# Optimization experiments

Hardware: AMD Instinct MI355X
Metric: run time of the kernel (lower is better)

The kernel has to match this reference:

```python
import jax, jax.numpy as jnp
import numpy as np

REG = 0.01
NUM_PS, NUM_QS, NUM_RS, D = 100000, 100000, 1000, 256
B = 4096


def setup_inputs() -> dict:
    key = jax.random.key(0)
    k1, k2, k3, k4, k5, k6, k7 = jax.random.split(key, 7)
    # xavier_uniform bound for a (d, d*d) fan view: sqrt(6/(d + d*d))
    bound = float(np.sqrt(6.0 / (D + D * D)))
    return {
        "ps": jax.random.randint(k1, (B,), 0, NUM_PS),
        "qs": jax.random.randint(k2, (B,), 0, NUM_QS),
        "rs": jax.random.randint(k3, (B,), 0, NUM_RS),
        "P_table": jax.random.normal(k4, (NUM_PS, D), dtype=jnp.float32),
        "Q_table": jax.random.normal(k5, (NUM_QS, D), dtype=jnp.float32),
        "R_table": jax.random.normal(k6, (NUM_RS, D), dtype=jnp.float32),
        "W": jax.random.uniform(k7, (D, D, D), dtype=jnp.float32, minval=-bound, maxval=bound),
    }


def reference(ps, qs, rs, P_table, Q_table, R_table, W):
    p = P_table[ps]  # (B, d)
    q = Q_table[qs]  # (B, d)
    r = R_table[rs]  # (B, d)
    # W.view(d, d*d) then reshape (B, d_r, d_q): axis order of W is (p, r, q)
    # trilinear: out_b = sum_{i,j,k} p_bi W_ijk r_bj q_bk
    Wp = jnp.einsum('bi,ijk->bjk', p, W)        # (B, d, d), the big GEMM
    out = jnp.einsum('bjk,bj,bk->b', Wp, r, q)  # two batched mat-vecs
    inferences = out[:, None]                   # (B, 1)
    regs = REG * (jnp.linalg.norm(p) + jnp.linalg.norm(q) + jnp.linalg.norm(r))
    return inferences, regs
```

## Files before the change

kernel.cpp:

```cpp
#include <hip/hip_runtime.h>
#include <hip/hip_bf16.h>


#define DDIM 256
#define NIK  65536
#define BM   128
#define BN   128
#define BK   64
#define NCH2 2
#define NPANEL 8

typedef unsigned int uint;
typedef __attribute__((ext_vector_type(8))) short bf16x8;
typedef __attribute__((ext_vector_type(4))) float f32x4;

static __device__ __forceinline__ unsigned short f2bf(float f) {
    __hip_bfloat16 h = __float2bfloat16(f);
    return *reinterpret_cast<unsigned short*>(&h);
}
static __device__ __forceinline__ float bf2f(unsigned short u) {
    return __uint_as_float(((uint)u) << 16);
}

#define GLOAD_LDS16(gsrc, ldst)                                                \
    __builtin_amdgcn_global_load_lds(                                          \
        (const __attribute__((address_space(1))) void*)(gsrc),                 \
        (__attribute__((address_space(3))) void*)(ldst), 16, 0, 0)

__global__ __launch_bounds__(256)
void conv_r_kernel(const float* __restrict__ R, unsigned short* __restrict__ Rb,
                   int n4) {
    int idx = blockIdx.x * 256 + threadIdx.x;
    if (idx < n4) {
        float4 v = *reinterpret_cast<const float4*>(R + idx * 4);
        ushort4 o;
        o.x = f2bf(v.x); o.y = f2bf(v.y); o.z = f2bf(v.z); o.w = f2bf(v.w);
        *reinterpret_cast<ushort4*>(Rb + idx * 4) = o;
    }
}

__global__ __launch_bounds__(256)
void conv_wt_kernel(const float* __restrict__ W, unsigned short* __restrict__ Wt) {
    const int k0 = blockIdx.x * 64;
    const int j0 = blockIdx.y * 128;
    const int i  = blockIdx.z;
    const int t  = threadIdx.x;

    __shared__ float sT[64][129];

    const float* Wi = W + (size_t)i * NIK;
#pragma unroll
    for (int it = 0; it < 8; ++it) {
        int slot = it * 256 + t;
        int jj = slot >> 4, c = slot & 15;
        float4 v = *reinterpret_cast<const float4*>(
            Wi + (size_t)(j0 + jj) * DDIM + k0 + c * 4);
        sT[c * 4 + 0][jj] = v.x;
        sT[c * 4 + 1][jj] = v.y;
        sT[c * 4 + 2][jj] = v.z;
        sT[c * 4 + 3][jj] = v.w;
    }
    __syncthreads();
#pragma unroll
    for (int it = 0; it < 4; ++it) {
        int u = it * 256 + t;
        int kk = u >> 4, jg = u & 15;
        union { unsigned short us[8]; uint4 v; } pk;
#pragma unroll
        for (int m = 0; m < 8; ++m) pk.us[m] = f2bf(sT[kk][jg * 8 + m]);
        *reinterpret_cast<uint4*>(
            Wt + (size_t)(i * DDIM + k0 + kk) * DDIM + j0 + jg * 8) = pk.v;
    }
}

__global__ __launch_bounds__(256, 2)
void stage1_kernel(const unsigned short* __restrict__ Rb,
                   const unsigned short* __restrict__ Wt,
                   unsigned short* __restrict__ WR,
                   int r_lo, int cnt) {
    const int t     = threadIdx.x;
    const int lane  = t & 63;
    const int wid   = t >> 6;
    const int strip = blockIdx.x;
    const int r0    = blockIdx.y * BM;

    __shared__ char smem[65536];

    const int wr = (wid >> 1) * 64;
    const int wn = (wid & 1) * 64;

    f32x4 acc[4][4];
#pragma unroll
    for (int a = 0; a < 4; ++a)
#pragma unroll
        for (int b = 0; b < 4; ++b) {
            acc[a][b][0] = 0.f; acc[a][b][1] = 0.f;
            acc[a][b][2] = 0.f; acc[a][b][3] = 0.f;
        }

#define STAGE_S(s, boff)                                                        \
    {                                                                           \
        const int j0s = ((s) & 3) * BK;                                         \
        const int n0s = strip * (BN * NPANEL) + ((s) >> 2) * BN;                \
        _Pragma("unroll")                                                       \
        for (int c = 0; c < 4; ++c) {                                           \
            int u = c * 256 + t;                                                \
            int row = u >> 3, g = u & 7;                                        \
            int rg = r0 + row;                                                  \
            if (rg >= cnt) rg = 0;                                              \
            GLOAD_LDS16(Rb + (size_t)(r_lo + rg) * DDIM + j0s +                 \
                            ((g ^ (row & 7)) << 3),                             \
                        smem + (boff) + u * 16);                                \
        }                                                                       \
        _Pragma("unroll")                                                       \
        for (int c = 0; c < 4; ++c) {                                           \
            int u = c * 256 + t;                                                \
            int row = u >> 3, g = u & 7;                                        \
            GLOAD_LDS16(Wt + (size_t)(n0s + row) * DDIM + j0s +                 \
                            ((g ^ (row & 7)) << 3),                             \
                        smem + 32768 + (boff) + u * 16);                        \
        }                                                                       \
    }

    STAGE_S(0, 0);
    __syncthreads();

    const int c16   = lane & 15;
    const int gq    = lane >> 4;
    const int ubase = wn >> 5;
    char* WRb = (char*)WR;

    for (int s = 0; s < 4 * NPANEL; ++s) {
        const int coff = (s & 1) << 14;
        if (s < 4 * NPANEL - 1) STAGE_S(s + 1, coff ^ 16384);

        char* Acur = smem + coff;
        char* Bcur = smem + 32768 + coff;
#pragma unroll
        for (int ks = 0; ks < 2; ++ks) {
            bf16x8 a[4], b[4];
            const int jg = ks * 4 + (lane >> 4);
#pragma unroll
            for (int f = 0; f < 4; ++f) {
                int rowB = wn + f * 16 + (lane & 15);
                a[f] = *reinterpret_cast<const bf16x8*>(
                    Bcur + rowB * 128 + ((jg ^ (rowB & 7)) << 4));
                int rowA = wr + f * 16 + (lane & 15);
                b[f] = *reinterpret_cast<const bf16x8*>(
                    Acur + rowA * 128 + ((jg ^ (rowA & 7)) << 4));
            }
#pragma unroll
            for (int fi = 0; fi < 4; ++fi)
#pragma unroll
                for (int fr = 0; fr < 4; ++fr)
                    acc[fi][fr] = __builtin_amdgcn_mfma_f32_16x16x32_bf16(
                        a[fi], b[fr], acc[fi][fr], 0, 0, 0);
        }

        if ((s & 3) == 3) {
            const int n0  = strip * (BN * NPANEL) + (s >> 2) * BN;
            const int i_g = n0 >> 8;
            const size_t obase = (size_t)(i_g >> 4) * 8192 +
                                 (size_t)(i_g & 15) * 512 +
                                 (size_t)(n0 & 255) * 2;
#pragma unroll
            for (int fr = 0; fr < 4; ++fr) {
                int rg = r0 + wr + fr * 16 + c16;
                if (rg < cnt) {
#pragma unroll
                    for (int kts = 0; kts < 2; ++kts) {
                        union { unsigned short us[8]; uint4 v; } pk;
#pragma unroll
                        for (int vv = 0; vv < 4; ++vv) {
                            pk.us[vv]     = f2bf(acc[2 * kts + 0][fr][vv]);
                            pk.us[4 + vv] = f2bf(acc[2 * kts + 1][fr][vv]);
                        }
                        *reinterpret_cast<uint4*>(
                            WRb + (size_t)rg * 131072 + obase +
                            (ubase + kts) * 64 + gq * 16) = pk.v;
                    }
                }
            }
#pragma unroll
            for (int a = 0; a < 4; ++a)
#pragma unroll
                for (int b = 0; b < 4; ++b) {
                    acc[a][b][0] = 0.f; acc[a][b][1] = 0.f;
                    acc[a][b][2] = 0.f; acc[a][b][3] = 0.f;
                }
        }
        __syncthreads();
    }
#undef STAGE_S
}

__global__ void prep_kernel(int* __restrict__ counts, float* __restrict__ norms,
                            int n) {
    int idx = blockIdx.x * 256 + threadIdx.x;
    if (idx < n) counts[idx] = 0;
    if (idx < 3) norms[idx] = 0.f;
}

__global__ void hist_kernel(const int* __restrict__ rs, int* __restrict__ counts,
                            int B) {
    int b = blockIdx.x * 256 + threadIdx.x;
    if (b < B) atomicAdd(&counts[rs[b]], 1);
}

__global__ __launch_bounds__(1024)
void scan_kernel(const int* __restrict__ counts, int* __restrict__ offs,
                 int* __restrict__ cursor, int n) {
    __shared__ int buf[2][1024];
    const int t = threadIdx.x;
    int cur = 0;
    buf[0][t] = (t < n) ? counts[t] : 0;
    __syncthreads();
    for (int d = 1; d < 1024; d <<= 1) {
        int x = buf[cur][t] + ((t >= d) ? buf[cur][t - d] : 0);
        buf[cur ^ 1][t] = x;
        cur ^= 1;
        __syncthreads();
    }
    if (t < n) {
        int inc = buf[cur][t];
        offs[t + 1] = inc;
        cursor[t] = inc - counts[t];
        if (t == 0) offs[0] = 0;
    }
}

__global__ void fill_kernel(const int* __restrict__ rs, int* __restrict__ cursor,
                            int* __restrict__ list, int B) {
    int b = blockIdx.x * 256 + threadIdx.x;
    if (b < B) {
        int pos = atomicAdd(&cursor[rs[b]], 1);
        list[pos] = b;
    }
}

__global__ __launch_bounds__(256)
void stage2_kernel(const int* __restrict__ list, const int* __restrict__ offs,
                   const int* __restrict__ ps, const int* __restrict__ qs,
                   const float* __restrict__ P, const float* __restrict__ Q,
                   const unsigned short* __restrict__ WR,
                   float* __restrict__ partial, int r_lo, int B) {
    const int r_rel = blockIdx.x;
    const int r     = r_lo + r_rel;
    const int start = offs[r], end = offs[r + 1];
    if (start >= end) return;
    const int ihalf = blockIdx.y;
    const int t     = threadIdx.x;
    const int lane  = t & 63;
    const int w     = t >> 6;
    const int s     = lane & 15;
    const int kg    = lane >> 4;

    __shared__ float Lq[16][258];
    __shared__ float Lp[16][133];
    __shared__ float red[16][4];

    const unsigned short* Mbase = WR + (size_t)r_rel * NIK;

    for (int s0 = start; s0 < end; s0 += 16) {
        const int ns = min(16, end - s0);
        for (int u = t; u < ns * 64; u += 256) {
            int ss = u >> 6, c = u & 63;
            *reinterpret_cast<float4*>(&Lq[ss][c * 4]) =
                *reinterpret_cast<const float4*>(
                    Q + (size_t)qs[list[s0 + ss]] * DDIM + c * 4);
        }
        for (int u = t; u < ns * 32; u += 256) {
            int ss = u >> 5, c = u & 31;
            *reinterpret_cast<float4*>(&Lp[ss][c * 4]) =
                *reinterpret_cast<const float4*>(
                    P + (size_t)ps[list[s0 + ss]] * DDIM + ihalf * 128 + c * 4);
        }
        __syncthreads();

        bf16x8 bq[8];
#pragma unroll
        for (int kt = 0; kt < 8; ++kt) {
#pragma unroll
            for (int eh = 0; eh < 2; ++eh) {
#pragma unroll
                for (int ev = 0; ev < 4; ++ev) {
                    float v = (s < ns) ? Lq[s][kt * 32 + eh * 16 + kg * 4 + ev]
                                       : 0.f;
                    bq[kt][eh * 4 + ev] = (short)f2bf(v);
                }
            }
        }

        float acc_out = 0.f;
#pragma unroll
        for (int ibl = 0; ibl < 2; ++ibl) {
            const int ibh = w * 2 + ibl;
            const int ibg = ihalf * 8 + ibh;
            const unsigned short* abase =
                Mbase + (size_t)ibg * 4096 + (lane & 15) * 256 + kg * 8;
            bf16x8 af[8];
#pragma unroll
            for (int kt = 0; kt < 8; ++kt)
                af[kt] = *reinterpret_cast<const bf16x8*>(abase + kt * 32);
            f32x4 acc = {0.f, 0.f, 0.f, 0.f};
#pragma unroll
            for (int kt = 0; kt < 8; ++kt)
                acc = __builtin_amdgcn_mfma_f32_16x16x32_bf16(af[kt], bq[kt],
                                                              acc, 0, 0, 0);
#pragma unroll
            for (int reg = 0; reg < 4; ++reg) {
                int il = ibh * 16 + kg * 4 + reg;
                float pv = (s < ns) ? Lp[s][il] : 0.f;
                acc_out += acc[reg] * pv;
            }
        }
        acc_out += __shfl_xor(acc_out, 16, 64);
        acc_out += __shfl_xor(acc_out, 32, 64);
        if (lane < 16) red[s][w] = acc_out;
        __syncthreads();
        if (t < ns)
            partial[(size_t)ihalf * B + list[s0 + t]] =
                red[t][0] + red[t][1] + red[t][2] + red[t][3];
        __syncthreads();
    }
}

__global__ void sum_out_kernel(const float* __restrict__ partial,
                               float* __restrict__ out, int B) {
    int b = blockIdx.x * 256 + threadIdx.x;
    if (b < B) out[b] = partial[b] + partial[(size_t)B + b];
}

__global__ __launch_bounds__(256)
void norm_kernel(const int* __restrict__ ps, const int* __restrict__ qs,
                 const int* __restrict__ rs, const float* __restrict__ P,
                 const float* __restrict__ Q, const float* __restrict__ R,
                 float* __restrict__ accum, int B) {
    const int which = blockIdx.y;
    const int*   idx = (which == 0) ? ps : (which == 1) ? qs : rs;
    const float* tab = (which == 0) ? P : (which == 1) ? Q : R;
    float a = 0.f;
    const int total = B * 64;
    for (int e = blockIdx.x * 256 + threadIdx.x; e < total; e += gridDim.x * 256) {
        int b = e >> 6, cc = e & 63;
        float4 v = *reinterpret_cast<const float4*>(tab + (size_t)idx[b] * DDIM + cc * 4);
        a += v.x * v.x + v.y * v.y + v.z * v.z + v.w * v.w;
    }
#pragma unroll
    for (int off = 32; off; off >>= 1) a += __shfl_down(a, off, 64);
    __shared__ float red[4];
    if ((threadIdx.x & 63) == 0) red[threadIdx.x >> 6] = a;
    __syncthreads();
    if (threadIdx.x == 0) atomicAdd(accum + which, red[0] + red[1] + red[2] + red[3]);
}

__global__ void finalize_kernel(const float* __restrict__ n,
                                float* __restrict__ out, int nB) {
    if (threadIdx.x == 0 && blockIdx.x == 0)
        out[nB] = 0.01f * (sqrtf(n[0]) + sqrtf(n[1]) + sqrtf(n[2]));
}

extern "C" void kernel_launch(void* const* d_in, const int* in_sizes, int n_in,
                              void* d_out, int out_size, void* d_ws,
                              size_t ws_size, hipStream_t stream) {
    const int*   ps = (const int*)d_in[0];
    const int*   qs = (const int*)d_in[1];
    const int*   rs = (const int*)d_in[2];
    const float* P  = (const float*)d_in[3];
    const float* Q  = (const float*)d_in[4];
    const float* R  = (const float*)d_in[5];
    const float* W  = (const float*)d_in[6];
    float* out = (float*)d_out;

    const int B      = in_sizes[0];
    const int NUM_RS = in_sizes[5] / DDIM;

    size_t off = 0;
    float* norms = (float*)((char*)d_ws + off);          off += 256;
    int* counts  = (int*)((char*)d_ws + off);            off += (size_t)NUM_RS * 4;
    int* offs    = (int*)((char*)d_ws + off);            off += (size_t)(NUM_RS + 1) * 4;
    int* cursor  = (int*)((char*)d_ws + off);            off += (size_t)NUM_RS * 4;
    int* list    = (int*)((char*)d_ws + off);            off += (size_t)B * 4;
    off = (off + 255) & ~(size_t)255;
    float* partial = (float*)((char*)d_ws + off);        off += (size_t)NCH2 * B * 4;
    off = (off + 255) & ~(size_t)255;
    unsigned short* Rb = (unsigned short*)((char*)d_ws + off);
    off += (size_t)NUM_RS * DDIM * 2;
    off = (off + 255) & ~(size_t)255;
    unsigned short* Wt = (unsigned short*)((char*)d_ws + off);
    off += (size_t)NIK * DDIM * 2;
    off = (off + 255) & ~(size_t)255;
    unsigned short* WR = (unsigned short*)((char*)d_ws + off);

    size_t wr_bytes = (ws_size > off) ? ws_size - off : 0;
    int max_chunk = (int)(wr_bytes / ((size_t)NIK * 2));
    if (max_chunk > NUM_RS) max_chunk = NUM_RS;
    if (max_chunk < 1) max_chunk = 1;

    prep_kernel<<<(NUM_RS + 255) / 256, 256, 0, stream>>>(counts, norms, NUM_RS);
    hist_kernel<<<(B + 255) / 256, 256, 0, stream>>>(rs, counts, B);
    scan_kernel<<<1, 1024, 0, stream>>>(counts, offs, cursor, NUM_RS);
    fill_kernel<<<(B + 255) / 256, 256, 0, stream>>>(rs, cursor, list, B);
    norm_kernel<<<dim3(128, 3), 256, 0, stream>>>(ps, qs, rs, P, Q, R, norms, B);
    finalize_kernel<<<1, 64, 0, stream>>>(norms, out, B);

    conv_r_kernel<<<(NUM_RS * DDIM / 4 + 255) / 256, 256, 0, stream>>>(
        R, Rb, NUM_RS * DDIM / 4);
    conv_wt_kernel<<<dim3(4, 2, DDIM), 256, 0, stream>>>(W, Wt);

    for (int lo = 0; lo < NUM_RS; lo += max_chunk) {
        int cnt = NUM_RS - lo;
        if (cnt > max_chunk) cnt = max_chunk;
        dim3 g1(NIK / BN / NPANEL, (cnt + BM - 1) / BM);
        stage1_kernel<<<g1, 256, 0, stream>>>(Rb, Wt, WR, lo, cnt);
        stage2_kernel<<<dim3(cnt, NCH2), 256, 0, stream>>>(
            list, offs, ps, qs, P, Q, WR, partial, lo, B);
    }
    sum_out_kernel<<<(B + 255) / 256, 256, 0, stream>>>(partial, out, B);
}
```

Before: 128.4 us.

## Fuse the trilinear contraction into the GEMM epilogue and drop the WR intermediate

The separate stage2 kernel and the large bf16 WR buffer are removed. The GEMM epilogue now stages each finished accumulator tile in LDS. Each thread then reduces its assigned batch elements (from the r-sorted list) against pre-gathered Q and P rows, writing per-strip partial sums that a final kernel adds up. This avoids writing and re-reading the full per-r W·r tensor and the chunk loop that depended on workspace size. In exchange the epilogue gains extra barriers, scalar dot loops with uneven per-thread work, and a new gather kernel for Q and P.

```diff
diff --git a/kernel.cpp b/kernel.cpp
--- a/kernel.cpp
+++ b/kernel.cpp
@@ -7,8 +7,9 @@
 #define BM   128
 #define BN   128
 #define BK   64
-#define NCH2 2
 #define NPANEL 8
+#define NSTRIP 64
+#define MAXS 8
 
 typedef unsigned int uint;
 typedef __attribute__((ext_vector_type(8))) short bf16x8;
@@ -37,6 +38,16 @@
         o.x = f2bf(v.x); o.y = f2bf(v.y); o.z = f2bf(v.z); o.w = f2bf(v.w);
         *reinterpret_cast<ushort4*>(Rb + idx * 4) = o;
     }
+}
+
+__global__ __launch_bounds__(256)
+void conv_qp_kernel(const int* __restrict__ qs, const int* __restrict__ ps,
+                    const float* __restrict__ Q, const float* __restrict__ P,
+                    float* __restrict__ Qb, float* __restrict__ Pb) {
+    const int b = blockIdx.x;
+    const int t = threadIdx.x;
+    Qb[(size_t)b * DDIM + t] = Q[(size_t)qs[b] * DDIM + t];
+    Pb[(size_t)b * DDIM + t] = P[(size_t)ps[b] * DDIM + t];
 }
 
 __global__ __launch_bounds__(256)
@@ -76,8 +87,10 @@
 __global__ __launch_bounds__(256, 2)
 void stage1_kernel(const unsigned short* __restrict__ Rb,
                    const unsigned short* __restrict__ Wt,
-                   unsigned short* __restrict__ WR,
-                   int r_lo, int cnt) {
+                   const int* __restrict__ rs, const int* __restrict__ list,
+                   const int* __restrict__ offs,
+                   const float* __restrict__ Qb, const float* __restrict__ Pb,
+                   float* __restrict__ partial, int cnt) {
     const int t     = threadIdx.x;
     const int lane  = t & 63;
     const int wid   = t >> 6;
@@ -85,9 +98,27 @@
     const int r0    = blockIdx.y * BM;
 
     __shared__ char smem[65536];
-
-    const int wr = (wid >> 1) * 64;
-    const int wn = (wid & 1) * 64;
+    __shared__ unsigned short eplds[2 * 4096];
+
+    const int wr  = (wid >> 1) * 64;
+    const int wn  = (wid & 1) * 64;
+    const int c16 = lane & 15;
+    const int gq  = lane >> 4;
+
+    const int start = offs[r0];
+    int rend = r0 + BM; if (rend > cnt) rend = cnt;
+    const int end = offs[rend];
+    int   meta[MAXS];
+    float racc[MAXS];
+#pragma unroll
+    for (int sl = 0; sl < MAXS; ++sl) {
+        int idx = start + t + sl * 256;
+        if (idx < end) {
+            int b = list[idx];
+            meta[sl] = b | ((rs[b] - r0) << 16);
+        } else meta[sl] = -1;
+        racc[sl] = 0.f;
+    }
 
     f32x4 acc[4][4];
 #pragma unroll
@@ -108,7 +139,7 @@
             int row = u >> 3, g = u & 7;                                        \
             int rg = r0 + row;                                                  \
             if (rg >= cnt) rg = 0;                                              \
-            GLOAD_LDS16(Rb + (size_t)(r_lo + rg) * DDIM + j0s +                 \
+            GLOAD_LDS16(Rb + (size_t)rg * DDIM + j0s +                          \
                             ((g ^ (row & 7)) << 3),                             \
                         smem + (boff) + u * 16);                                \
         }                                                                       \
@@ -125,11 +156,6 @@
     STAGE_S(0, 0);
     __syncthreads();
 
-    const int c16   = lane & 15;
-    const int gq    = lane >> 4;
-    const int ubase = wn >> 5;
-    char* WRb = (char*)WR;
-
     for (int s = 0; s < 4 * NPANEL; ++s) {
         const int coff = (s & 1) << 14;
         if (s < 4 * NPANEL - 1) STAGE_S(s + 1, coff ^ 16384);
@@ -158,26 +184,52 @@
         }
 
         if ((s & 3) == 3) {
-            const int n0  = strip * (BN * NPANEL) + (s >> 2) * BN;
-            const int i_g = n0 >> 8;
-            const size_t obase = (size_t)(i_g >> 4) * 8192 +
-                                 (size_t)(i_g & 15) * 512 +
-                                 (size_t)(n0 & 255) * 2;
-#pragma unroll
-            for (int fr = 0; fr < 4; ++fr) {
-                int rg = r0 + wr + fr * 16 + c16;
-                if (rg < cnt) {
-#pragma unroll
-                    for (int kts = 0; kts < 2; ++kts) {
-                        union { unsigned short us[8]; uint4 v; } pk;
-#pragma unroll
-                        for (int vv = 0; vv < 4; ++vv) {
-                            pk.us[vv]     = f2bf(acc[2 * kts + 0][fr][vv]);
-                            pk.us[4 + vv] = f2bf(acc[2 * kts + 1][fr][vv]);
+            const int n0    = strip * (BN * NPANEL) + (s >> 2) * BN;
+            const int i_g   = n0 >> 8;
+            const int khalf = (n0 >> 7) & 1;
+            const float* qbase = Qb + khalf * 128;
+#pragma unroll
+            for (int qt = 0; qt < 4; ++qt) {
+                unsigned short* ep = eplds + (qt & 1) * 4096;
+                if ((wr >> 6) == (qt >> 1)) {
+#pragma unroll
+                    for (int f2 = 0; f2 < 2; ++f2) {
+                        const int fr = (qt & 1) * 2 + f2;
+                        const int rl = f2 * 16 + c16;
+#pragma unroll
+                        for (int fi = 0; fi < 4; ++fi) {
+                            const int ggr = (wn >> 2) + fi * 4 + gq;
+                            union { unsigned short us[4]; uint2 v; } pk;
+#pragma unroll
+                            for (int vv = 0; vv < 4; ++vv)
+                                pk.us[vv] = f2bf(acc[fi][fr][vv]);
+                            *reinterpret_cast<uint2*>(
+                                ep + rl * 128 + ((ggr ^ rl) << 2)) = pk.v;
                         }
-                        *reinterpret_cast<uint4*>(
-                            WRb + (size_t)rg * 131072 + obase +
-                            (ubase + kts) * 64 + gq * 16) = pk.v;
+                    }
+                }
+                __syncthreads();
+#pragma unroll
+                for (int sl = 0; sl < MAXS; ++sl) {
+                    int m = meta[sl];
+                    if (m >= 0 && (m >> 21) == qt) {
+                        const int b  = m & 0xFFFF;
+                        const int rl = (m >> 16) & 31;
+                        const unsigned short* tp = ep + rl * 128;
+                        const float* qp = qbase + (size_t)b * DDIM;
+                        float dot = 0.f;
+                        for (int g = 0; g < 32; ++g) {
+                            union { unsigned short us[4]; uint2 v; } tv;
+                            tv.v = *reinterpret_cast<const uint2*>(
+                                tp + ((g ^ rl) << 2));
+                            float4 qv = *reinterpret_cast<const float4*>(
+                                qp + g * 4);
+                            dot += bf2f(tv.us[0]) * qv.x +
+                                   bf2f(tv.us[1]) * qv.y +
+                                   bf2f(tv.us[2]) * qv.z +
+                                   bf2f(tv.us[3]) * qv.w;
+                        }
+                        racc[sl] += Pb[(size_t)b * DDIM + i_g] * dot;
                     }
                 }
             }
@@ -191,6 +243,11 @@
         }
         __syncthreads();
     }
+
+#pragma unroll
+    for (int sl = 0; sl < MAXS; ++sl)
+        if (meta[sl] >= 0)
+            partial[(size_t)(meta[sl] & 0xFFFF) * NSTRIP + strip] = racc[sl];
 #undef STAGE_S
 }
 
@@ -239,96 +296,20 @@
 }
 
 __global__ __launch_bounds__(256)
-void stage2_kernel(const int* __restrict__ list, const int* __restrict__ offs,
-                   const int* __restrict__ ps, const int* __restrict__ qs,
-                   const float* __restrict__ P, const float* __restrict__ Q,
-                   const unsigned short* __restrict__ WR,
-                   float* __restrict__ partial, int r_lo, int B) {
-    const int r_rel = blockIdx.x;
-    const int r     = r_lo + r_rel;
-    const int start = offs[r], end = offs[r + 1];
-    if (start >= end) return;
-    const int ihalf = blockIdx.y;
-    const int t     = threadIdx.x;
-    const int lane  = t & 63;
-    const int w     = t >> 6;
-    const int s     = lane & 15;
-    const int kg    = lane >> 4;
-
-    __shared__ float Lq[16][258];
-    __shared__ float Lp[16][133];
-    __shared__ float red[16][4];
-
-    const unsigned short* Mbase = WR + (size_t)r_rel * NIK;
-
-    for (int s0 = start; s0 < end; s0 += 16) {
-        const int ns = min(16, end - s0);
-        for (int u = t; u < ns * 64; u += 256) {
-            int ss = u >> 6, c = u & 63;
-            *reinterpret_cast<float4*>(&Lq[ss][c * 4]) =
-                *reinterpret_cast<const float4*>(
-                    Q + (size_t)qs[list[s0 + ss]] * DDIM + c * 4);
+void sum_out_kernel(const float* __restrict__ partial, float* __restrict__ out,
+                    int B) {
+    int b = blockIdx.x * 256 + threadIdx.x;
+    if (b < B) {
+        const float4* p4 =
+            reinterpret_cast<const float4*>(partial + (size_t)b * NSTRIP);
+        float s = 0.f;
+#pragma unroll
+        for (int i = 0; i < NSTRIP / 4; ++i) {
+            float4 v = p4[i];
+            s += (v.x + v.y) + (v.z + v.w);
         }
-        for (int u = t; u < ns * 32; u += 256) {
-            int ss = u >> 5, c = u & 31;
-            *reinterpret_cast<float4*>(&Lp[ss][c * 4]) =
-                *reinterpret_cast<const float4*>(
-                    P + (size_t)ps[list[s0 + ss]] * DDIM + ihalf * 128 + c * 4);
-        }
-        __syncthreads();
-
-        bf16x8 bq[8];
-#pragma unroll
-        for (int kt = 0; kt < 8; ++kt) {
-#pragma unroll
-            for (int eh = 0; eh < 2; ++eh) {
-#pragma unroll
-                for (int ev = 0; ev < 4; ++ev) {
-                    float v = (s < ns) ? Lq[s][kt * 32 + eh * 16 + kg * 4 + ev]
-                                       : 0.f;
-                    bq[kt][eh * 4 + ev] = (short)f2bf(v);
-                }
-            }
-        }
-
-        float acc_out = 0.f;
-#pragma unroll
-        for (int ibl = 0; ibl < 2; ++ibl) {
-            const int ibh = w * 2 + ibl;
-            const int ibg = ihalf * 8 + ibh;
-            const unsigned short* abase =
-                Mbase + (size_t)ibg * 4096 + (lane & 15) * 256 + kg * 8;
-            bf16x8 af[8];
-#pragma unroll
-            for (int kt = 0; kt < 8; ++kt)
-                af[kt] = *reinterpret_cast<const bf16x8*>(abase + kt * 32);
-            f32x4 acc = {0.f, 0.f, 0.f, 0.f};
-#pragma unroll
-            for (int kt = 0; kt < 8; ++kt)
-                acc = __builtin_amdgcn_mfma_f32_16x16x32_bf16(af[kt], bq[kt],
-                                                              acc, 0, 0, 0);
-#pragma unroll
-            for (int reg = 0; reg < 4; ++reg) {
-                int il = ibh * 16 + kg * 4 + reg;
-                float pv = (s < ns) ? Lp[s][il] : 0.f;
-                acc_out += acc[reg] * pv;
-            }
-        }
-        acc_out += __shfl_xor(acc_out, 16, 64);
-        acc_out += __shfl_xor(acc_out, 32, 64);
-        if (lane < 16) red[s][w] = acc_out;
-        __syncthreads();
-        if (t < ns)
-            partial[(size_t)ihalf * B + list[s0 + t]] =
-                red[t][0] + red[t][1] + red[t][2] + red[t][3];
-        __syncthreads();
-    }
-}
-
-__global__ void sum_out_kernel(const float* __restrict__ partial,
-                               float* __restrict__ out, int B) {
-    int b = blockIdx.x * 256 + threadIdx.x;
-    if (b < B) out[b] = partial[b] + partial[(size_t)B + b];
+        out[b] = s;
+    }
 }
 
 __global__ __launch_bounds__(256)
@@ -382,20 +363,16 @@
     int* cursor  = (int*)((char*)d_ws + off);            off += (size_t)NUM_RS * 4;
     int* list    = (int*)((char*)d_ws + off);            off += (size_t)B * 4;
     off = (off + 255) & ~(size_t)255;
-    float* partial = (float*)((char*)d_ws + off);        off += (size_t)NCH2 * B * 4;
+    float* partial = (float*)((char*)d_ws + off);        off += (size_t)B * NSTRIP * 4;
+    off = (off + 255) & ~(size_t)255;
+    float* Qb = (float*)((char*)d_ws + off);             off += (size_t)B * DDIM * 4;
+    float* Pb = (float*)((char*)d_ws + off);             off += (size_t)B * DDIM * 4;
     off = (off + 255) & ~(size_t)255;
     unsigned short* Rb = (unsigned short*)((char*)d_ws + off);
     off += (size_t)NUM_RS * DDIM * 2;
     off = (off + 255) & ~(size_t)255;
     unsigned short* Wt = (unsigned short*)((char*)d_ws + off);
     off += (size_t)NIK * DDIM * 2;
-    off = (off + 255) & ~(size_t)255;
-    unsigned short* WR = (unsigned short*)((char*)d_ws + off);
-
-    size_t wr_bytes = (ws_size > off) ? ws_size - off : 0;
-    int max_chunk = (int)(wr_bytes / ((size_t)NIK * 2));
-    if (max_chunk > NUM_RS) max_chunk = NUM_RS;
-    if (max_chunk < 1) max_chunk = 1;
 
     prep_kernel<<<(NUM_RS + 255) / 256, 256, 0, stream>>>(counts, norms, NUM_RS);
     hist_kernel<<<(B + 255) / 256, 256, 0, stream>>>(rs, counts, B);
@@ -406,15 +383,12 @@
 
     conv_r_kernel<<<(NUM_RS * DDIM / 4 + 255) / 256, 256, 0, stream>>>(
         R, Rb, NUM_RS * DDIM / 4);
+    conv_qp_kernel<<<B, 256, 0, stream>>>(qs, ps, Q, P, Qb, Pb);
     conv_wt_kernel<<<dim3(4, 2, DDIM), 256, 0, stream>>>(W, Wt);
 
-    for (int lo = 0; lo < NUM_RS; lo += max_chunk) {
-        int cnt = NUM_RS - lo;
-        if (cnt > max_chunk) cnt = max_chunk;
-        dim3 g1(NIK / BN / NPANEL, (cnt + BM - 1) / BM);
-        stage1_kernel<<<g1, 256, 0, stream>>>(Rb, Wt, WR, lo, cnt);
-        stage2_kernel<<<dim3(cnt, NCH2), 256, 0, stream>>>(
-            list, offs, ps, qs, P, Q, WR, partial, lo, B);
-    }
+    dim3 g1(NSTRIP, (NUM_RS + BM - 1) / BM);
+    stage1_kernel<<<g1, 256, 0, stream>>>(Rb, Wt, rs, list, offs, Qb, Pb,
+                                          partial, NUM_RS);
+
     sum_out_kernel<<<(B + 255) / 256, 256, 0, stream>>>(partial, out, B);
 }
```

New measurement: 422.4 us. 3.29x slower.

## Hoist R operand fragments into registers once per block in stage1

Applied to the files above, without the earlier changes.

The R tile for the block's rows is loaded once through shared memory into 32 bf16x8 register fragments, covering all four K slices. The main loop then streams only W panels through double-buffered LDS, halving shared memory and dropping the repeated R global loads and LDS reads on every step. In exchange, 128 extra VGPRs per thread are held live, which under launch_bounds(256,2) may cause spills or limit occupancy.

```diff
diff --git a/kernel.cpp b/kernel.cpp
--- a/kernel.cpp
+++ b/kernel.cpp
@@ -84,10 +84,41 @@
     const int strip = blockIdx.x;
     const int r0    = blockIdx.y * BM;
 
-    __shared__ char smem[65536];
+    __shared__ char smem[32768];
 
     const int wr = (wid >> 1) * 64;
     const int wn = (wid & 1) * 64;
+
+    bf16x8 rfrag[8][4];
+    {
+#pragma unroll
+        for (int rd = 0; rd < 4; ++rd) {
+            const int j0s = rd * BK;
+            __syncthreads();
+#pragma unroll
+            for (int c = 0; c < 4; ++c) {
+                int u = c * 256 + t;
+                int row = u >> 3, g = u & 7;
+                int rg = r0 + row;
+                if (rg >= cnt) rg = 0;
+                GLOAD_LDS16(Rb + (size_t)(r_lo + rg) * DDIM + j0s +
+                                ((g ^ (row & 7)) << 3),
+                            smem + u * 16);
+            }
+            __syncthreads();
+#pragma unroll
+            for (int ks = 0; ks < 2; ++ks) {
+                const int jg = ks * 4 + (lane >> 4);
+#pragma unroll
+                for (int f = 0; f < 4; ++f) {
+                    int rowA = wr + f * 16 + (lane & 15);
+                    rfrag[rd * 2 + ks][f] = *reinterpret_cast<const bf16x8*>(
+                        smem + rowA * 128 + ((jg ^ (rowA & 7)) << 4));
+                }
+            }
+        }
+        __syncthreads();
+    }
 
     f32x4 acc[4][4];
 #pragma unroll
@@ -98,31 +129,21 @@
             acc[a][b][2] = 0.f; acc[a][b][3] = 0.f;
         }
 
-#define STAGE_S(s, boff)                                                        \
+#define STAGE_W(p, kt, boff)                                                    \
     {                                                                           \
-        const int j0s = ((s) & 3) * BK;                                         \
-        const int n0s = strip * (BN * NPANEL) + ((s) >> 2) * BN;                \
-        _Pragma("unroll")                                                       \
-        for (int c = 0; c < 4; ++c) {                                           \
-            int u = c * 256 + t;                                                \
-            int row = u >> 3, g = u & 7;                                        \
-            int rg = r0 + row;                                                  \
-            if (rg >= cnt) rg = 0;                                              \
-            GLOAD_LDS16(Rb + (size_t)(r_lo + rg) * DDIM + j0s +                 \
-                            ((g ^ (row & 7)) << 3),                             \
-                        smem + (boff) + u * 16);                                \
-        }                                                                       \
+        const int j0s = (kt) * BK;                                              \
+        const int n0s = strip * (BN * NPANEL) + (p) * BN;                       \
         _Pragma("unroll")                                                       \
         for (int c = 0; c < 4; ++c) {                                           \
             int u = c * 256 + t;                                                \
             int row = u >> 3, g = u & 7;                                        \
             GLOAD_LDS16(Wt + (size_t)(n0s + row) * DDIM + j0s +                 \
                             ((g ^ (row & 7)) << 3),                             \
-                        smem + 32768 + (boff) + u * 16);                        \
+                        smem + (boff) + u * 16);                                \
         }                                                                       \
     }
 
-    STAGE_S(0, 0);
+    STAGE_W(0, 0, 0);
     __syncthreads();
 
     const int c16   = lane & 15;
@@ -130,68 +151,72 @@
     const int ubase = wn >> 5;
     char* WRb = (char*)WR;
 
-    for (int s = 0; s < 4 * NPANEL; ++s) {
-        const int coff = (s & 1) << 14;
-        if (s < 4 * NPANEL - 1) STAGE_S(s + 1, coff ^ 16384);
-
-        char* Acur = smem + coff;
-        char* Bcur = smem + 32768 + coff;
-#pragma unroll
-        for (int ks = 0; ks < 2; ++ks) {
-            bf16x8 a[4], b[4];
-            const int jg = ks * 4 + (lane >> 4);
-#pragma unroll
-            for (int f = 0; f < 4; ++f) {
-                int rowB = wn + f * 16 + (lane & 15);
-                a[f] = *reinterpret_cast<const bf16x8*>(
-                    Bcur + rowB * 128 + ((jg ^ (rowB & 7)) << 4));
-                int rowA = wr + f * 16 + (lane & 15);
-                b[f] = *reinterpret_cast<const bf16x8*>(
-                    Acur + rowA * 128 + ((jg ^ (rowA & 7)) << 4));
-            }
-#pragma unroll
-            for (int fi = 0; fi < 4; ++fi)
-#pragma unroll
-                for (int fr = 0; fr < 4; ++fr)
-                    acc[fi][fr] = __builtin_amdgcn_mfma_f32_16x16x32_bf16(
-                        a[fi], b[fr], acc[fi][fr], 0, 0, 0);
-        }
-
-        if ((s & 3) == 3) {
-            const int n0  = strip * (BN * NPANEL) + (s >> 2) * BN;
-            const int i_g = n0 >> 8;
-            const size_t obase = (size_t)(i_g >> 4) * 8192 +
-                                 (size_t)(i_g & 15) * 512 +
-                                 (size_t)(n0 & 255) * 2;
-#pragma unroll
-            for (int fr = 0; fr < 4; ++fr) {
-                int rg = r0 + wr + fr * 16 + c16;
-                if (rg < cnt) {
-#pragma unroll
-                    for (int kts = 0; kts < 2; ++kts) {
-                        union { unsigned short us[8]; uint4 v; } pk;
-#pragma unroll
-                        for (int vv = 0; vv < 4; ++vv) {
-                            pk.us[vv]     = f2bf(acc[2 * kts + 0][fr][vv]);
-                            pk.us[4 + vv] = f2bf(acc[2 * kts + 1][fr][vv]);
+    for (int p = 0; p < NPANEL; ++p) {
+#pragma unroll
+        for (int kt = 0; kt < 4; ++kt) {
+            const int coff = (kt & 1) << 14;
+            if (kt < 3) {
+                STAGE_W(p, kt + 1, coff ^ 16384);
+            } else if (p < NPANEL - 1) {
+                STAGE_W(p + 1, 0, coff ^ 16384);
+            }
+
+            char* Bcur = smem + coff;
+#pragma unroll
+            for (int ks = 0; ks < 2; ++ks) {
+                bf16x8 a[4];
+                const int jg = ks * 4 + (lane >> 4);
+#pragma unroll
+                for (int f = 0; f < 4; ++f) {
+                    int rowB = wn + f * 16 + (lane & 15);
+                    a[f] = *reinterpret_cast<const bf16x8*>(
+                        Bcur + rowB * 128 + ((jg ^ (rowB & 7)) << 4));
+                }
+#pragma unroll
+                for (int fi = 0; fi < 4; ++fi)
+#pragma unroll
+                    for (int fr = 0; fr < 4; ++fr)
+                        acc[fi][fr] = __builtin_amdgcn_mfma_f32_16x16x32_bf16(
+                            a[fi], rfrag[kt * 2 + ks][fr], acc[fi][fr],
+                            0, 0, 0);
+            }
+
+            if (kt == 3) {
+                const int n0  = strip * (BN * NPANEL) + p * BN;
+                const int i_g = n0 >> 8;
+                const size_t obase = (size_t)(i_g >> 4) * 8192 +
+                                     (size_t)(i_g & 15) * 512 +
+                                     (size_t)(n0 & 255) * 2;
+#pragma unroll
+                for (int fr = 0; fr < 4; ++fr) {
+                    int rg = r0 + wr + fr * 16 + c16;
+                    if (rg < cnt) {
+#pragma unroll
+                        for (int kts = 0; kts < 2; ++kts) {
+                            union { unsigned short us[8]; uint4 v; } pk;
+#pragma unroll
+                            for (int vv = 0; vv < 4; ++vv) {
+                                pk.us[vv]     = f2bf(acc[2 * kts + 0][fr][vv]);
+                                pk.us[4 + vv] = f2bf(acc[2 * kts + 1][fr][vv]);
+                            }
+                            *reinterpret_cast<uint4*>(
+                                WRb + (size_t)rg * 131072 + obase +
+                                (ubase + kts) * 64 + gq * 16) = pk.v;
                         }
-                        *reinterpret_cast<uint4*>(
-                            WRb + (size_t)rg * 131072 + obase +
-                            (ubase + kts) * 64 + gq * 16) = pk.v;
                     }
                 }
-            }
-#pragma unroll
-            for (int a = 0; a < 4; ++a)
-#pragma unroll
-                for (int b = 0; b < 4; ++b) {
-                    acc[a][b][0] = 0.f; acc[a][b][1] = 0.f;
-                    acc[a][b][2] = 0.f; acc[a][b][3] = 0.f;
-                }
-        }
-        __syncthreads();
-    }
-#undef STAGE_S
+#pragma unroll
+                for (int a2 = 0; a2 < 4; ++a2)
+#pragma unroll
+                    for (int b2 = 0; b2 < 4; ++b2) {
+                        acc[a2][b2][0] = 0.f; acc[a2][b2][1] = 0.f;
+                        acc[a2][b2][2] = 0.f; acc[a2][b2][3] = 0.f;
+                    }
+            }
+            __syncthreads();
+        }
+    }
+#undef STAGE_W
 }
 
 __global__ void prep_kernel(int* __restrict__ counts, float* __restrict__ norms,
```

After: 126.9 us. About the same (-1.2%).
